# Kernel optimization log

Measured on AMD Instinct MI355X. Metric: run time of the kernel, lower is better.

## Reference

```python
import jax, jax.numpy as jnp
import numpy as np
from functools import partial

B = 1024          # batch of VRP instances
N_CUST = 100      # customers
N = N_CUST + 1    # nodes incl. depot (node 0)
E = 128           # embed_dim
H = 8             # n_heads
DH = E // H       # head depth
CLIP = 10.0
T = 2 * N         # fixed number of decode steps (env.n_nodes * 2)


def setup_inputs() -> dict:
    key = jax.random.key(0)
    ks = jax.random.split(key, 11)
    s = E ** -0.5
    return {
        "depot_xy": jax.random.uniform(ks[0], (B, 2), dtype=jnp.float32),
        "customer_xy": jax.random.uniform(ks[1], (B, N_CUST, 2), dtype=jnp.float32),
        # demands normalized by vehicle capacity (1..9 / 50 for VRP100)
        "demand": jax.random.uniform(ks[2], (B, N_CUST), dtype=jnp.float32, minval=0.02, maxval=0.18),
        "node_embeddings": jax.random.normal(ks[3], (B, N, E), dtype=jnp.float32),
        "graph_embedding": jax.random.normal(ks[4], (B, E), dtype=jnp.float32),
        "Wk1": jax.random.normal(ks[5], (E, E), dtype=jnp.float32) * s,
        "Wv": jax.random.normal(ks[6], (E, E), dtype=jnp.float32) * s,
        "Wk2": jax.random.normal(ks[7], (E, E), dtype=jnp.float32) * s,
        "Wq_fixed": jax.random.normal(ks[8], (E, E), dtype=jnp.float32) * s,
        "Wout": jax.random.normal(ks[9], (E, E), dtype=jnp.float32) * s,
        "Wq_step": jax.random.normal(ks[10], (E + 1, E), dtype=jnp.float32) * s,
    }


def _decode(depot_xy, customer_xy, demand, node_embeddings, graph_embedding,
            Wk1, Wv, Wk2, Wq_fixed, Wout, Wq_step):
    # ---- compute_static ----
    Q_fixed = jnp.einsum('be,ef->bf', graph_embedding, Wq_fixed)[:, None, :]  # [B,1,E]
    K1 = jnp.einsum('bne,ef->bnf', node_embeddings, Wk1)                      # [B,N,E]
    V  = jnp.einsum('bne,ef->bnf', node_embeddings, Wv)
    K2 = jnp.einsum('bne,ef->bnf', node_embeddings, Wk2)
    K1h = K1.reshape(B, N, H, DH)
    Vh  = V.reshape(B, N, H, DH)
    inv_sqrt_dh = 1.0 / np.sqrt(DH)
    inv_sqrt_e = 1.0 / np.sqrt(E)
    bidx = jnp.arange(B)
    NEG = jnp.float32(-1e9)

    def step(carry, _):
        mask, D, prev_node, visited = carry
        # step_context = [embedding of current node, remaining capacity D]
        prev_emb = node_embeddings[bidx, prev_node]                 # [B,E]
        step_context = jnp.concatenate([prev_emb, D], axis=-1)[:, None, :]  # [B,1,E+1]
        # ---- compute_dynamic ----
        Q1 = Q_fixed + jnp.einsum('bqc,cf->bqf', step_context, Wq_step)      # [B,1,E]
        Q1h = Q1.reshape(B, 1, H, DH)
        scores = jnp.einsum('bqhd,bkhd->bhqk', Q1h, K1h) * inv_sqrt_dh       # [B,H,1,N]
        scores = jnp.where(mask[:, None, None, :], NEG, scores)
        attn = jax.nn.softmax(scores, axis=-1)
        glimpse = jnp.einsum('bhqk,bkhd->bqhd', attn, Vh).reshape(B, 1, E)
        Q2 = jnp.einsum('bqe,ef->bqf', glimpse, Wout)                        # [B,1,E]
        logits = CLIP * jnp.tanh(jnp.einsum('bqe,bke->bqk', Q2, K2) * inv_sqrt_e)
        logits = jnp.where(mask[:, None, :], NEG, logits)[:, 0]             # [B,N]
        log_p = jax.nn.log_softmax(logits, axis=-1)
        next_node = jnp.argmax(log_p, axis=-1)                               # greedy decode
        # ---- env._get_step ----
        is_depot = next_node == 0
        cust = jnp.clip(next_node - 1, 0, N_CUST - 1)
        sel_dem = jnp.where(is_depot, 0.0, demand[bidx, cust])
        D_new = jnp.where(is_depot[:, None], 1.0, D - sel_dem[:, None])      # refill at depot
        sel_onehot = (jnp.arange(N_CUST)[None, :] == cust[:, None]) & (~is_depot[:, None])
        visited = visited | sel_onehot
        mask_cust = visited | (demand > D_new)                               # visited or too big
        all_visited = jnp.all(visited, axis=-1)
        mask_depot = is_depot & (~all_visited)                               # can't stay at depot
        mask = jnp.concatenate([mask_depot[:, None], mask_cust], axis=-1)
        return (mask, D_new, next_node, visited), (log_p, next_node)

    mask0 = jnp.concatenate([jnp.ones((B, 1), bool), jnp.zeros((B, N_CUST), bool)], axis=-1)
    D0 = jnp.ones((B, 1), jnp.float32)
    prev0 = jnp.zeros((B,), jnp.int32)
    visited0 = jnp.zeros((B, N_CUST), bool)
    _, (log_ps, tours) = jax.lax.scan(step, (mask0, D0, prev0, visited0), None, length=T)
    log_ps = jnp.transpose(log_ps, (1, 0, 2))   # [B,T,N]
    tours = jnp.transpose(tours, (1, 0))        # [B,T]

    # ---- get_costs ----
    coords = jnp.concatenate([depot_xy[:, None, :], customer_xy], axis=1)    # [B,N,2]
    d = coords[bidx[:, None], tours]                                         # [B,T,2]
    def seglen(v):
        return jnp.sqrt(jnp.sum(v * v, axis=-1) + 1e-10)
    cost = (seglen(d[:, 1:] - d[:, :-1]).sum(-1)
            + seglen(d[:, 0] - depot_xy) + seglen(d[:, -1] - depot_xy))
    # ---- get_log_likelihood ----
    ll = jnp.take_along_axis(log_ps, tours[..., None], axis=-1)[..., 0].sum(-1)
    return cost, ll


def reference(depot_xy, customer_xy, demand, node_embeddings, graph_embedding,
              Wk1, Wv, Wk2, Wq_fixed, Wout, Wq_step):
    return _decode(depot_xy, customer_xy, demand, node_embeddings, graph_embedding,
                   Wk1, Wv, Wk2, Wq_fixed, Wout, Wq_step)
```

## Files before the change

kernel.cpp:

```cpp
#include <hip/hip_runtime.h>
#include <math.h>

#define B_   1024
#define NC   100
#define NN   101
#define E_   128
#define T_   202
#define SVP  132
#define NEGV   -1.0e9
#define GAPTHR 1.0e-3f
#define INVSQE 0.08838834764831845f
#define INVSQED 0.08838834764831845

__device__ __forceinline__ float rdlane(float v, int l) {
    return __int_as_float(__builtin_amdgcn_readlane(__float_as_int(v), l));
}
__device__ __forceinline__ float fast_tanh(float x) {
    float xc = fminf(fmaxf(x, -15.f), 15.f);
    float e  = __expf(2.f * xc);
    return (e - 1.f) / (e + 1.f);
}

__global__ void k_weights(const float* __restrict__ Wk2,
                          const float* __restrict__ Wout,
                          double* __restrict__ M64,
                          float* __restrict__ M32) {
    int g = blockIdx.x;
    int e = threadIdx.x;
    const float* w2 = Wk2 + g * E_;
    const float* wo = Wout + e * E_;
    double acc = 0.0;
#pragma unroll 8
    for (int f = 0; f < E_; ++f) acc += (double)w2[f] * (double)wo[f];
    M64[g * E_ + e] = acc;
    M32[g * E_ + e] = (float)acc;
}

__global__ __launch_bounds__(512, 2)
void k_decode(const float* __restrict__ depot_xy,
              const float* __restrict__ customer_xy,
              const float* __restrict__ demand,
              const float* __restrict__ node_emb,
              const float* __restrict__ graph_emb,
              const float* __restrict__ Wk1,
              const float* __restrict__ Wv,
              const float* __restrict__ Wq_fixed,
              const float* __restrict__ Wq_step,
              const double* __restrict__ M64,
              const float* __restrict__ M32,
              float* __restrict__ out)
{
    __shared__ float  sKs[NN * E_];
    __shared__ __align__(16) float sV[104 * SVP];
    __shared__ double sU[2224];
    __shared__ double sQfix64[E_];
    __shared__ double sWqD64[E_];
    __shared__ float  sQfix32[E_];
    __shared__ float  sWqD32[E_];
    __shared__ float  sCoord[2 * NN];
    __shared__ float  sDem[NC];
    __shared__ float  sD;
    __shared__ double sCost, sLL;
    __shared__ float  sPosX, sPosY;
    __shared__ int    sPrev, sMaskDepot, sTrig, sOvf;
    __shared__ unsigned long long sVis0, sVis1;

    float* fSc  = (float*)sU;
    float* fPx8 = (float*)sU + 832;
    double* dUZ = sU;
    double* dSc = sU + 1024;
    double* dQ1 = sU + 1832;
    double* dGl = sU + 1960;
    double* dVg = sU + 2088;

    const int b      = blockIdx.x;
    const int tid    = threadIdx.x;
    const int lane   = tid & 63;
    const int h      = __builtin_amdgcn_readfirstlane(tid >> 6);
    const int k1     = lane + 64;

    const float* emb = node_emb + (size_t)b * NN * E_;

    if (tid < E_) {
        const float* ge = graph_emb + (size_t)b * E_;
        double acc = 0.0;
        for (int g = 0; g < E_; ++g)
            acc += (double)ge[g] * (double)Wq_fixed[g * E_ + tid];
        sQfix64[tid] = acc;
        sQfix32[tid] = (float)acc;
        sWqD64[tid]  = (double)Wq_step[128 * E_ + tid];
        sWqD32[tid]  = Wq_step[128 * E_ + tid];
    }
    if (tid < 2 * NN) {
        int k = tid >> 1, xy = tid & 1;
        sCoord[tid] = (k == 0) ? depot_xy[(size_t)b * 2 + xy]
                               : customer_xy[((size_t)b * NC + (k - 1)) * 2 + xy];
    }
    if (tid < NC) sDem[tid] = demand[(size_t)b * NC + tid];
    if (tid == 0) {
        sD = 1.f; sPrev = 0; sVis0 = 0ull; sVis1 = 0ull;
        sMaskDepot = 1; sCost = 0.0; sLL = 0.0; sTrig = 0; sOvf = 0;
        sPosX = depot_xy[(size_t)b * 2 + 0];
        sPosY = depot_xy[(size_t)b * 2 + 1];
    }
    for (int i = tid; i < 3 * SVP; i += 512) sV[101 * SVP + i] = 0.f;

    for (int idx = tid; idx < NN * 32; idx += 512) {
        int k  = idx >> 5;
        int e4 = (idx & 31) * 4;
        const float* er = emb + (size_t)k * E_;
        float4 aV = {0.f, 0.f, 0.f, 0.f};
        float4 aK = {0.f, 0.f, 0.f, 0.f};
        for (int g = 0; g < E_; ++g) {
            float eg = er[g];
            float4 wv = *(const float4*)(Wv      + (size_t)g * E_ + e4);
            float4 wq = *(const float4*)(Wq_step + (size_t)g * E_ + e4);
            aV.x += eg * wv.x; aV.y += eg * wv.y;
            aV.z += eg * wv.z; aV.w += eg * wv.w;
            aK.x += eg * wq.x; aK.y += eg * wq.y;
            aK.z += eg * wq.z; aK.w += eg * wq.w;
        }
        *(float4*)(sV  + (size_t)k * SVP + e4) = aV;
        *(float4*)(sKs + (size_t)k * E_  + e4) = aK;
    }

    float rA[32], rK2[32];
#pragma unroll
    for (int j = 0; j < 32; ++j) { rA[j] = 0.f; rK2[j] = 0.f; }
    {
        const float* er0 = emb + (size_t)lane * E_;
        const float* er1 = emb + (size_t)((k1 < NN) ? k1 : lane) * E_;
        const float  e1s = (k1 < NN) ? 1.f : 0.f;
        const float* w1b = Wk1 + h * 16;
        const float* m2b = M32 + h * 16;
        for (int g = 0; g < E_; ++g) {
            float a0 = er0[g];
            float a1 = er1[g] * e1s;
            const float* w1 = w1b + (size_t)g * E_;
            const float* mm = m2b + (size_t)g * E_;
#pragma unroll
            for (int d = 0; d < 16; ++d) {
                rA[d]       += a0 * w1[d];
                rA[16 + d]  += a1 * w1[d];
                rK2[d]      += a0 * mm[d];
                rK2[16 + d] += a1 * mm[d];
            }
        }
    }
    __syncthreads();

    for (int t = 0; t < T_; ++t) {
        {
            int prev = sPrev;
            float Dv = sD;
            int d_ = h * 16 + (lane & 15);
            float q1v = (sQfix32[d_] + sKs[(size_t)prev * E_ + d_]
                         + Dv * sWqD32[d_]) * 0.25f;

            unsigned long long v0 = sVis0, v1 = sVis1;
            bool mk0, mk1;
            if (lane == 0) mk0 = (sMaskDepot != 0);
            else {
                int c = lane - 1;
                mk0 = ((v0 >> c) & 1ull) || (sDem[c] > Dv);
            }
            if (k1 < NN) {
                int c = k1 - 1;
                bool vis = (c < 64) ? ((v0 >> c) & 1ull)
                                    : ((v1 >> (c - 64)) & 1ull);
                mk1 = vis || (sDem[c] > Dv);
            } else mk1 = true;

            float s0a = 0.f, s0b = 0.f, s1a = 0.f, s1b = 0.f;
#pragma unroll
            for (int d = 0; d < 8; ++d) {
                float qd = rdlane(q1v, d);
                s0a += rA[d] * qd;
                s1a += rA[16 + d] * qd;
            }
#pragma unroll
            for (int d = 8; d < 16; ++d) {
                float qd = rdlane(q1v, d);
                s0b += rA[d] * qd;
                s1b += rA[16 + d] * qd;
            }
            float s0 = s0a + s0b, s1 = s1a + s1b;
            bool ovf = (!mk0 && s0 > 80.f) || (!mk1 && s1 > 80.f);
            if (__any(ovf)) { if (lane == 0) sOvf = 1; }
            float w0 = mk0 ? 0.f : __expf(fminf(s0, 80.f));
            float w1 = mk1 ? 0.f : __expf(fminf(s1, 80.f));
            fSc[h * 104 + lane] = w0;
            if (k1 < 104) fSc[h * 104 + k1] = w1;

            __builtin_amdgcn_wave_barrier();

            int cq4 = lane >> 4;
            const float* sc = fSc + h * 104 + cq4 * 26;
            const float* vv = sV + (size_t)(cq4 * 26) * SVP + d_;
            float p = 0.f, ssum = 0.f;
#pragma unroll
            for (int j = 0; j < 26; ++j) {
                float wgt = sc[j];
                p    += wgt * vv[(size_t)j * SVP];
                ssum += wgt;
            }
            p    += __shfl_xor(p, 16);
            ssum += __shfl_xor(ssum, 16);
            p    += __shfl_xor(p, 32);
            ssum += __shfl_xor(ssum, 32);
            float glval = p * (1.0f / ssum);

            float x0 = 0.f, x1 = 0.f;
#pragma unroll
            for (int d = 0; d < 16; ++d) {
                float gd = rdlane(glval, d);
                x0 += rK2[d] * gd;
                x1 += rK2[16 + d] * gd;
            }
            fPx8[h * E_ + lane] = x0;
            if (k1 < NN) fPx8[h * E_ + k1] = x1;
        }
        __syncthreads();

        if (tid < 64) {
            int kA = tid, kB = tid + 64;
            float xA = 0.f, xB = -3.0e38f;
#pragma unroll
            for (int hh = 0; hh < 8; ++hh) xA += fPx8[hh * E_ + kA];
            xA *= INVSQE;
            bool mk1;
            if (kA == 0) mk1 = (sMaskDepot != 0);
            else {
                int c = kA - 1;
                bool vis = (c < 64) ? ((sVis0 >> c) & 1ull) : ((sVis1 >> (c - 64)) & 1ull);
                mk1 = vis || (sDem[c] > sD);
            }
            bool mk2 = true;
            if (kB < NN) {
                float xs = 0.f;
#pragma unroll
                for (int hh = 0; hh < 8; ++hh) xs += fPx8[hh * E_ + kB];
                xB = xs * INVSQE;
                int c = kB - 1;
                bool vis = (c < 64) ? ((sVis0 >> c) & 1ull) : ((sVis1 >> (c - 64)) & 1ull);
                mk2 = vis || (sDem[c] > sD);
            }
            float a1v = mk1 ? -3.0e38f : xA;
            float a2v = mk2 ? -3.0e38f : xB;
            float m1; int mi;
            if (a2v > a1v) { m1 = a2v; mi = kB; }
            else           { m1 = a1v; mi = kA; }
            float ls = 0.f;
            if (!mk1)              ls += __expf(10.f * fast_tanh(xA));
            if (kB < NN && !mk2)   ls += __expf(10.f * fast_tanh(xB));
#pragma unroll
            for (int off = 32; off > 0; off >>= 1) {
                float om1 = __shfl_xor(m1, off);
                int   omi = __shfl_xor(mi, off);
                ls += __shfl_xor(ls, off);
                if (om1 > m1 || (om1 == m1 && omi < mi)) { m1 = om1; mi = omi; }
            }
            bool near = false;
            if (!mk1 && kA != mi && a1v > m1 - GAPTHR) near = true;
            if (!mk2 && kB != mi && a2v > m1 - GAPTHR) near = true;
            bool trigAny = __any(near);
            if (tid == 0) {
                bool trig = trigAny || (sOvf != 0) || !(m1 == m1);
                sOvf = 0;
                if (trig) {
                    sTrig = 1;
                } else {
                    float lsel = 10.f * fast_tanh(m1);
                    float logp = lsel - __logf(ls);
                    int nxt = mi;
                    sLL += (double)logp;
                    bool isdep = (nxt == 0);
                    if (isdep) {
                        sD = 1.0f;
                    } else {
                        int c = nxt - 1;
                        sD = sD - sDem[c];
                        if (c < 64) sVis0 |= (1ull << c);
                        else        sVis1 |= (1ull << (c - 64));
                    }
                    bool allv = (sVis0 == 0xFFFFFFFFFFFFFFFFull) &&
                                (sVis1 == 0x0000000FFFFFFFFFull);
                    sMaskDepot = (isdep && !allv) ? 1 : 0;
                    sPrev = nxt;
                    float cx = sCoord[2 * nxt], cy = sCoord[2 * nxt + 1];
                    double dx = (double)cx - (double)sPosX;
                    double dy = (double)cy - (double)sPosY;
                    sCost += sqrt(dx * dx + dy * dy + 1e-10);
                    sPosX = cx; sPosY = cy;
                }
            }
        }
        __syncthreads();

        if (sTrig) {
            if (tid < E_) {
                const float* ep = emb + (size_t)sPrev * E_;
                double ks = 0.0;
                for (int g = 0; g < E_; ++g)
                    ks += (double)ep[g] * (double)Wq_step[(size_t)g * E_ + tid];
                dQ1[tid] = (sQfix64[tid] + ks + (double)sD * sWqD64[tid]) * 0.25;
            }
            __syncthreads();
            for (int idx = tid; idx < 1024; idx += 512) {
                int g = idx >> 3, hh = idx & 7;
                double u = 0.0;
#pragma unroll 4
                for (int d = 0; d < 16; ++d)
                    u += dQ1[hh * 16 + d] * (double)Wk1[(size_t)g * E_ + hh * 16 + d];
                dUZ[idx] = u;
            }
            __syncthreads();
            for (int idx = tid; idx < 1024; idx += 512) {
                int k = idx & 127, hh = idx >> 7;
                if (k < NN) {
                    bool mk;
                    if (k == 0) mk = (sMaskDepot != 0);
                    else {
                        int c = k - 1;
                        bool vis = (c < 64) ? ((sVis0 >> c) & 1ull) : ((sVis1 >> (c - 64)) & 1ull);
                        mk = vis || (sDem[c] > sD);
                    }
                    if (mk) dSc[hh * NN + k] = NEGV;
                    else {
                        const float* ek = emb + (size_t)k * E_;
                        double s = 0.0;
                        for (int g = 0; g < E_; ++g)
                            s += (double)ek[g] * dUZ[g * 8 + hh];
                        dSc[hh * NN + k] = s;
                    }
                }
            }
            __syncthreads();
            {
                int hh = tid >> 6, ln = tid & 63;
                int kA = ln, kB = ln + 64;
                double v1 = dSc[hh * NN + kA];
                double v2 = (kB < NN) ? dSc[hh * NN + kB] : -1.0e300;
                double m = fmax(v1, v2);
#pragma unroll
                for (int off = 32; off > 0; off >>= 1)
                    m = fmax(m, __shfl_xor(m, off));
                double e1 = exp(v1 - m);
                double e2 = (kB < NN) ? exp(v2 - m) : 0.0;
                double s = e1 + e2;
#pragma unroll
                for (int off = 32; off > 0; off >>= 1)
                    s += __shfl_xor(s, off);
                double inv = 1.0 / s;
                dSc[hh * NN + kA] = e1 * inv;
                if (kB < NN) dSc[hh * NN + kB] = e2 * inv;
            }
            __syncthreads();
            for (int idx = tid; idx < 1024; idx += 512) {
                int g = idx >> 3, hh = idx & 7;
                double z = 0.0;
                for (int k = 0; k < NN; ++k)
                    z += dSc[hh * NN + k] * (double)emb[(size_t)k * E_ + g];
                dUZ[idx] = z;
            }
            __syncthreads();
            if (tid < E_) {
                int hh = tid >> 4;
                double g2 = 0.0;
                for (int g = 0; g < E_; ++g)
                    g2 += dUZ[g * 8 + hh] * (double)Wv[(size_t)g * E_ + tid];
                dGl[tid] = g2;
            }
            __syncthreads();
            if (tid < E_) {
                double v = 0.0;
                for (int e = 0; e < E_; ++e)
                    v += dGl[e] * M64[(size_t)tid * E_ + e];
                dVg[tid] = v;
            }
            __syncthreads();
            if (tid < NN) {
                const float* ek = emb + (size_t)tid * E_;
                double x = 0.0;
                for (int g = 0; g < E_; ++g)
                    x += (double)ek[g] * dVg[g];
                dQ1[tid] = x * INVSQED;
            }
            __syncthreads();
            if (tid < 64) {
                int kA = tid, kB = tid + 64;
                double x1 = dQ1[kA];
                bool mk1;
                if (kA == 0) mk1 = (sMaskDepot != 0);
                else {
                    int c = kA - 1;
                    bool vis = (c < 64) ? ((sVis0 >> c) & 1ull) : ((sVis1 >> (c - 64)) & 1ull);
                    mk1 = vis || (sDem[c] > sD);
                }
                double x2 = 0.0; bool mk2 = true;
                if (kB < NN) {
                    x2 = dQ1[kB];
                    int c = kB - 1;
                    bool vis = (c < 64) ? ((sVis0 >> c) & 1ull) : ((sVis1 >> (c - 64)) & 1ull);
                    mk2 = vis || (sDem[c] > sD);
                }
                double a1 = mk1 ? -1.0e300 : x1;
                double a2 = (kB < NN && !mk2) ? x2 : -1.0e300;
                double mv; int mi;
                if (a1 >= a2) { mv = a1; mi = kA; } else { mv = a2; mi = kB; }
#pragma unroll
                for (int off = 32; off > 0; off >>= 1) {
                    double ov = __shfl_xor(mv, off);
                    int    oi = __shfl_xor(mi, off);
                    if (ov > mv || (ov == mv && oi < mi)) { mv = ov; mi = oi; }
                }
                double lmax = 10.0 * tanh(mv);
                double l1 = mk1 ? NEGV : 10.0 * tanh(x1);
                double l2 = (kB < NN) ? (mk2 ? NEGV : 10.0 * tanh(x2)) : 0.0;
                double s = exp(l1 - lmax) + ((kB < NN) ? exp(l2 - lmax) : 0.0);
#pragma unroll
                for (int off = 32; off > 0; off >>= 1)
                    s += __shfl_xor(s, off);
                if (tid == 0) {
                    int nxt = mi;
                    sLL += -log(s);
                    bool isdep = (nxt == 0);
                    if (isdep) {
                        sD = 1.0f;
                    } else {
                        int c = nxt - 1;
                        sD = sD - sDem[c];
                        if (c < 64) sVis0 |= (1ull << c);
                        else        sVis1 |= (1ull << (c - 64));
                    }
                    bool allv = (sVis0 == 0xFFFFFFFFFFFFFFFFull) &&
                                (sVis1 == 0x0000000FFFFFFFFFull);
                    sMaskDepot = (isdep && !allv) ? 1 : 0;
                    sPrev = nxt;
                    float cx = sCoord[2 * nxt], cy = sCoord[2 * nxt + 1];
                    double dx = (double)cx - (double)sPosX;
                    double dy = (double)cy - (double)sPosY;
                    sCost += sqrt(dx * dx + dy * dy + 1e-10);
                    sPosX = cx; sPosY = cy;
                    sTrig = 0;
                }
            }
            __syncthreads();
        }
    }

    if (tid == 0) {
        double dx = (double)sCoord[0] - (double)sPosX;
        double dy = (double)sCoord[1] - (double)sPosY;
        out[b]      = (float)(sCost + sqrt(dx * dx + dy * dy + 1e-10));
        out[B_ + b] = (float)sLL;
    }
}

extern "C" void kernel_launch(void* const* d_in, const int* in_sizes, int n_in,
                              void* d_out, int out_size, void* d_ws, size_t ws_size,
                              hipStream_t stream) {
    const float* depot = (const float*)d_in[0];
    const float* cust  = (const float*)d_in[1];
    const float* dem   = (const float*)d_in[2];
    const float* nemb  = (const float*)d_in[3];
    const float* gemb  = (const float*)d_in[4];
    const float* Wk1   = (const float*)d_in[5];
    const float* Wv    = (const float*)d_in[6];
    const float* Wk2   = (const float*)d_in[7];
    const float* Wqf   = (const float*)d_in[8];
    const float* Wout  = (const float*)d_in[9];
    const float* Wqs   = (const float*)d_in[10];
    float*  out = (float*)d_out;
    double* M64 = (double*)d_ws;
    float*  M32 = (float*)((char*)d_ws + 131072);

    k_weights<<<dim3(128), dim3(128), 0, stream>>>(Wk2, Wout, M64, M32);
    k_decode <<<dim3(B_),  dim3(512), 0, stream>>>(depot, cust, dem, nemb, gemb,
                                                   Wk1, Wv, Wqf, Wqs, M64, M32, out);
}
```

Before: 3.130 ms.

## Replicate decode state in registers and drop per-step barrier via double buffering

Every wave now redundantly computes the argmax/selection and keeps the decode state (capacity, visited bits, prev node, cost, log-likelihood) in registers, instead of wave 0 updating shared memory and all waves re-reading it after a second barrier. Per-step partial logits and overflow flags are double-buffered by step parity, so each step needs only one __syncthreads on the fast path. The slow fp64 fallback is kept, now nested inside the branch, with state copied to and from shared memory. The trade is redundant selection work in all eight waves and a larger reduction per wave, in exchange for removing a block-wide barrier and the shared-memory state round trip each step.

```diff
diff --git a/kernel.cpp b/kernel.cpp
--- a/kernel.cpp
+++ b/kernel.cpp
@@ -62,22 +62,23 @@
     __shared__ float  sD;
     __shared__ double sCost, sLL;
     __shared__ float  sPosX, sPosY;
-    __shared__ int    sPrev, sMaskDepot, sTrig, sOvf;
+    __shared__ int    sPrev, sMaskDepot, sTrig;
     __shared__ unsigned long long sVis0, sVis1;
 
     float* fSc  = (float*)sU;
-    float* fPx8 = (float*)sU + 832;
+    float* fPxD = (float*)sU + 832;
+    int*   sOvfA = (int*)((float*)sU + 2880);
     double* dUZ = sU;
     double* dSc = sU + 1024;
     double* dQ1 = sU + 1832;
     double* dGl = sU + 1960;
     double* dVg = sU + 2088;
 
-    const int b      = blockIdx.x;
-    const int tid    = threadIdx.x;
-    const int lane   = tid & 63;
-    const int h      = __builtin_amdgcn_readfirstlane(tid >> 6);
-    const int k1     = lane + 64;
+    const int b    = blockIdx.x;
+    const int tid  = threadIdx.x;
+    const int lane = tid & 63;
+    const int h    = __builtin_amdgcn_readfirstlane(tid >> 6);
+    const int k1   = lane + 64;
 
     const float* emb = node_emb + (size_t)b * NN * E_;
 
@@ -97,12 +98,7 @@
                                : customer_xy[((size_t)b * NC + (k - 1)) * 2 + xy];
     }
     if (tid < NC) sDem[tid] = demand[(size_t)b * NC + tid];
-    if (tid == 0) {
-        sD = 1.f; sPrev = 0; sVis0 = 0ull; sVis1 = 0ull;
-        sMaskDepot = 1; sCost = 0.0; sLL = 0.0; sTrig = 0; sOvf = 0;
-        sPosX = depot_xy[(size_t)b * 2 + 0];
-        sPosY = depot_xy[(size_t)b * 2 + 1];
-    }
+    if (tid == 0) sTrig = 0;
     for (int i = tid; i < 3 * SVP; i += 512) sV[101 * SVP + i] = 0.f;
 
     for (int idx = tid; idx < NN * 32; idx += 512) {
@@ -147,27 +143,33 @@
             }
         }
     }
+
+    float  rD = 1.0f;
+    int    rPrev = 0, rMaskDep = 1;
+    unsigned long long rV0 = 0ull, rV1 = 0ull;
+    double rCost = 0.0, rLL = 0.0;
+    float  rPx = depot_xy[(size_t)b * 2 + 0];
+    float  rPy = depot_xy[(size_t)b * 2 + 1];
     __syncthreads();
 
     for (int t = 0; t < T_; ++t) {
+        const int bsel = t & 1;
         {
-            int prev = sPrev;
-            float Dv = sD;
+            float Dv = rD;
             int d_ = h * 16 + (lane & 15);
-            float q1v = (sQfix32[d_] + sKs[(size_t)prev * E_ + d_]
+            float q1v = (sQfix32[d_] + sKs[(size_t)rPrev * E_ + d_]
                          + Dv * sWqD32[d_]) * 0.25f;
 
-            unsigned long long v0 = sVis0, v1 = sVis1;
             bool mk0, mk1;
-            if (lane == 0) mk0 = (sMaskDepot != 0);
+            if (lane == 0) mk0 = (rMaskDep != 0);
             else {
                 int c = lane - 1;
-                mk0 = ((v0 >> c) & 1ull) || (sDem[c] > Dv);
+                mk0 = ((rV0 >> c) & 1ull) || (sDem[c] > Dv);
             }
             if (k1 < NN) {
                 int c = k1 - 1;
-                bool vis = (c < 64) ? ((v0 >> c) & 1ull)
-                                    : ((v1 >> (c - 64)) & 1ull);
+                bool vis = (c < 64) ? ((rV0 >> c) & 1ull)
+                                    : ((rV1 >> (c - 64)) & 1ull);
                 mk1 = vis || (sDem[c] > Dv);
             } else mk1 = true;
 
@@ -186,7 +188,8 @@
             }
             float s0 = s0a + s0b, s1 = s1a + s1b;
             bool ovf = (!mk0 && s0 > 80.f) || (!mk1 && s1 > 80.f);
-            if (__any(ovf)) { if (lane == 0) sOvf = 1; }
+            int wOvf = __any(ovf) ? 1 : 0;
+            if (lane == 0) sOvfA[bsel * 8 + h] = wOvf;
             float w0 = mk0 ? 0.f : __expf(fminf(s0, 80.f));
             float w1 = mk1 ? 0.f : __expf(fminf(s1, 80.f));
             fSc[h * 104 + lane] = w0;
@@ -217,34 +220,40 @@
                 x0 += rK2[d] * gd;
                 x1 += rK2[16 + d] * gd;
             }
-            fPx8[h * E_ + lane] = x0;
-            if (k1 < NN) fPx8[h * E_ + k1] = x1;
+            float* px = fPxD + bsel * 1024 + h * E_;
+            px[lane] = x0;
+            if (k1 < NN) px[k1] = x1;
         }
         __syncthreads();
 
-        if (tid < 64) {
-            int kA = tid, kB = tid + 64;
-            float xA = 0.f, xB = -3.0e38f;
-#pragma unroll
-            for (int hh = 0; hh < 8; ++hh) xA += fPx8[hh * E_ + kA];
+        {
+            int kA = lane, kB = k1;
+            const float* px = fPxD + bsel * 1024;
+            float xA = 0.f;
+#pragma unroll
+            for (int hh = 0; hh < 8; ++hh) xA += px[hh * E_ + kA];
             xA *= INVSQE;
             bool mk1;
-            if (kA == 0) mk1 = (sMaskDepot != 0);
+            if (kA == 0) mk1 = (rMaskDep != 0);
             else {
                 int c = kA - 1;
-                bool vis = (c < 64) ? ((sVis0 >> c) & 1ull) : ((sVis1 >> (c - 64)) & 1ull);
-                mk1 = vis || (sDem[c] > sD);
-            }
-            bool mk2 = true;
+                bool vis = (c < 64) ? ((rV0 >> c) & 1ull) : ((rV1 >> (c - 64)) & 1ull);
+                mk1 = vis || (sDem[c] > rD);
+            }
+            float xB = -3.0e38f; bool mk2 = true;
             if (kB < NN) {
                 float xs = 0.f;
 #pragma unroll
-                for (int hh = 0; hh < 8; ++hh) xs += fPx8[hh * E_ + kB];
+                for (int hh = 0; hh < 8; ++hh) xs += px[hh * E_ + kB];
                 xB = xs * INVSQE;
                 int c = kB - 1;
-                bool vis = (c < 64) ? ((sVis0 >> c) & 1ull) : ((sVis1 >> (c - 64)) & 1ull);
-                mk2 = vis || (sDem[c] > sD);
-            }
+                bool vis = (c < 64) ? ((rV0 >> c) & 1ull) : ((rV1 >> (c - 64)) & 1ull);
+                mk2 = vis || (sDem[c] > rD);
+            }
+            int oa = 0;
+#pragma unroll
+            for (int hh = 0; hh < 8; ++hh) oa |= sOvfA[bsel * 8 + hh];
+
             float a1v = mk1 ? -3.0e38f : xA;
             float a2v = mk2 ? -3.0e38f : xB;
             float m1; int mi;
@@ -264,196 +273,199 @@
             if (!mk1 && kA != mi && a1v > m1 - GAPTHR) near = true;
             if (!mk2 && kB != mi && a2v > m1 - GAPTHR) near = true;
             bool trigAny = __any(near);
-            if (tid == 0) {
-                bool trig = trigAny || (sOvf != 0) || !(m1 == m1);
-                sOvf = 0;
-                if (trig) {
+            bool trig = trigAny || (oa != 0) || !(m1 == m1);
+
+            if (!trig) {
+                int nxt = mi;
+                float lsel = 10.f * fast_tanh(m1);
+                float logp = lsel - __logf(ls);
+                rLL += (double)logp;
+                bool isdep = (nxt == 0);
+                if (isdep) {
+                    rD = 1.0f;
+                } else {
+                    int c = nxt - 1;
+                    rD = rD - sDem[c];
+                    if (c < 64) rV0 |= (1ull << c);
+                    else        rV1 |= (1ull << (c - 64));
+                }
+                bool allv = (rV0 == 0xFFFFFFFFFFFFFFFFull) &&
+                            (rV1 == 0x0000000FFFFFFFFFull);
+                rMaskDep = (isdep && !allv) ? 1 : 0;
+                rPrev = nxt;
+                float cx = sCoord[2 * nxt], cy = sCoord[2 * nxt + 1];
+                double dx = (double)cx - (double)rPx;
+                double dy = (double)cy - (double)rPy;
+                rCost += sqrt(dx * dx + dy * dy + 1e-10);
+                rPx = cx; rPy = cy;
+            } else {
+                if (tid == 0) {
+                    sD = rD; sPrev = rPrev; sMaskDepot = rMaskDep;
+                    sVis0 = rV0; sVis1 = rV1;
+                    sCost = rCost; sLL = rLL; sPosX = rPx; sPosY = rPy;
                     sTrig = 1;
-                } else {
-                    float lsel = 10.f * fast_tanh(m1);
-                    float logp = lsel - __logf(ls);
-                    int nxt = mi;
-                    sLL += (double)logp;
-                    bool isdep = (nxt == 0);
-                    if (isdep) {
-                        sD = 1.0f;
-                    } else {
-                        int c = nxt - 1;
-                        sD = sD - sDem[c];
-                        if (c < 64) sVis0 |= (1ull << c);
-                        else        sVis1 |= (1ull << (c - 64));
+                }
+                __syncthreads();
+                if (tid < E_) {
+                    const float* ep = emb + (size_t)sPrev * E_;
+                    double ks = 0.0;
+                    for (int g = 0; g < E_; ++g)
+                        ks += (double)ep[g] * (double)Wq_step[(size_t)g * E_ + tid];
+                    dQ1[tid] = (sQfix64[tid] + ks + (double)sD * sWqD64[tid]) * 0.25;
+                }
+                __syncthreads();
+                for (int idx = tid; idx < 1024; idx += 512) {
+                    int g = idx >> 3, hh = idx & 7;
+                    double u = 0.0;
+#pragma unroll 4
+                    for (int d = 0; d < 16; ++d)
+                        u += dQ1[hh * 16 + d] * (double)Wk1[(size_t)g * E_ + hh * 16 + d];
+                    dUZ[idx] = u;
+                }
+                __syncthreads();
+                for (int idx = tid; idx < 1024; idx += 512) {
+                    int k = idx & 127, hh = idx >> 7;
+                    if (k < NN) {
+                        bool mk;
+                        if (k == 0) mk = (sMaskDepot != 0);
+                        else {
+                            int c = k - 1;
+                            bool vis = (c < 64) ? ((sVis0 >> c) & 1ull) : ((sVis1 >> (c - 64)) & 1ull);
+                            mk = vis || (sDem[c] > sD);
+                        }
+                        if (mk) dSc[hh * NN + k] = NEGV;
+                        else {
+                            const float* ek = emb + (size_t)k * E_;
+                            double s = 0.0;
+                            for (int g = 0; g < E_; ++g)
+                                s += (double)ek[g] * dUZ[g * 8 + hh];
+                            dSc[hh * NN + k] = s;
+                        }
                     }
-                    bool allv = (sVis0 == 0xFFFFFFFFFFFFFFFFull) &&
-                                (sVis1 == 0x0000000FFFFFFFFFull);
-                    sMaskDepot = (isdep && !allv) ? 1 : 0;
-                    sPrev = nxt;
-                    float cx = sCoord[2 * nxt], cy = sCoord[2 * nxt + 1];
-                    double dx = (double)cx - (double)sPosX;
-                    double dy = (double)cy - (double)sPosY;
-                    sCost += sqrt(dx * dx + dy * dy + 1e-10);
-                    sPosX = cx; sPosY = cy;
-                }
+                }
+                __syncthreads();
+                {
+                    int hh = tid >> 6, ln = tid & 63;
+                    int kA2 = ln, kB2 = ln + 64;
+                    double v1 = dSc[hh * NN + kA2];
+                    double v2 = (kB2 < NN) ? dSc[hh * NN + kB2] : -1.0e300;
+                    double m = fmax(v1, v2);
+#pragma unroll
+                    for (int off = 32; off > 0; off >>= 1)
+                        m = fmax(m, __shfl_xor(m, off));
+                    double e1 = exp(v1 - m);
+                    double e2 = (kB2 < NN) ? exp(v2 - m) : 0.0;
+                    double s = e1 + e2;
+#pragma unroll
+                    for (int off = 32; off > 0; off >>= 1)
+                        s += __shfl_xor(s, off);
+                    double inv = 1.0 / s;
+                    dSc[hh * NN + kA2] = e1 * inv;
+                    if (kB2 < NN) dSc[hh * NN + kB2] = e2 * inv;
+                }
+                __syncthreads();
+                for (int idx = tid; idx < 1024; idx += 512) {
+                    int g = idx >> 3, hh = idx & 7;
+                    double z = 0.0;
+                    for (int k = 0; k < NN; ++k)
+                        z += dSc[hh * NN + k] * (double)emb[(size_t)k * E_ + g];
+                    dUZ[idx] = z;
+                }
+                __syncthreads();
+                if (tid < E_) {
+                    int hh = tid >> 4;
+                    double g2 = 0.0;
+                    for (int g = 0; g < E_; ++g)
+                        g2 += dUZ[g * 8 + hh] * (double)Wv[(size_t)g * E_ + tid];
+                    dGl[tid] = g2;
+                }
+                __syncthreads();
+                if (tid < E_) {
+                    double v = 0.0;
+                    for (int e = 0; e < E_; ++e)
+                        v += dGl[e] * M64[(size_t)tid * E_ + e];
+                    dVg[tid] = v;
+                }
+                __syncthreads();
+                if (tid < NN) {
+                    const float* ek = emb + (size_t)tid * E_;
+                    double x = 0.0;
+                    for (int g = 0; g < E_; ++g)
+                        x += (double)ek[g] * dVg[g];
+                    dQ1[tid] = x * INVSQED;
+                }
+                __syncthreads();
+                if (tid < 64) {
+                    int kA2 = tid, kB2 = tid + 64;
+                    double x1 = dQ1[kA2];
+                    bool fk1;
+                    if (kA2 == 0) fk1 = (sMaskDepot != 0);
+                    else {
+                        int c = kA2 - 1;
+                        bool vis = (c < 64) ? ((sVis0 >> c) & 1ull) : ((sVis1 >> (c - 64)) & 1ull);
+                        fk1 = vis || (sDem[c] > sD);
+                    }
+                    double x2 = 0.0; bool fk2 = true;
+                    if (kB2 < NN) {
+                        x2 = dQ1[kB2];
+                        int c = kB2 - 1;
+                        bool vis = (c < 64) ? ((sVis0 >> c) & 1ull) : ((sVis1 >> (c - 64)) & 1ull);
+                        fk2 = vis || (sDem[c] > sD);
+                    }
+                    double a1 = fk1 ? -1.0e300 : x1;
+                    double a2 = (kB2 < NN && !fk2) ? x2 : -1.0e300;
+                    double mv; int fmi;
+                    if (a1 >= a2) { mv = a1; fmi = kA2; } else { mv = a2; fmi = kB2; }
+#pragma unroll
+                    for (int off = 32; off > 0; off >>= 1) {
+                        double ov = __shfl_xor(mv, off);
+                        int    oi = __shfl_xor(fmi, off);
+                        if (ov > mv || (ov == mv && oi < fmi)) { mv = ov; fmi = oi; }
+                    }
+                    double lmax = 10.0 * tanh(mv);
+                    double l1 = fk1 ? NEGV : 10.0 * tanh(x1);
+                    double l2 = (kB2 < NN) ? (fk2 ? NEGV : 10.0 * tanh(x2)) : 0.0;
+                    double s = exp(l1 - lmax) + ((kB2 < NN) ? exp(l2 - lmax) : 0.0);
+#pragma unroll
+                    for (int off = 32; off > 0; off >>= 1)
+                        s += __shfl_xor(s, off);
+                    if (tid == 0) {
+                        int nxt = fmi;
+                        sLL += -log(s);
+                        bool isdep = (nxt == 0);
+                        if (isdep) {
+                            sD = 1.0f;
+                        } else {
+                            int c = nxt - 1;
+                            sD = sD - sDem[c];
+                            if (c < 64) sVis0 |= (1ull << c);
+                            else        sVis1 |= (1ull << (c - 64));
+                        }
+                        bool allv = (sVis0 == 0xFFFFFFFFFFFFFFFFull) &&
+                                    (sVis1 == 0x0000000FFFFFFFFFull);
+                        sMaskDepot = (isdep && !allv) ? 1 : 0;
+                        sPrev = nxt;
+                        float cx = sCoord[2 * nxt], cy = sCoord[2 * nxt + 1];
+                        double dx = (double)cx - (double)sPosX;
+                        double dy = (double)cy - (double)sPosY;
+                        sCost += sqrt(dx * dx + dy * dy + 1e-10);
+                        sPosX = cx; sPosY = cy;
+                        sTrig = 0;
+                    }
+                }
+                __syncthreads();
+                rD = sD; rPrev = sPrev; rMaskDep = sMaskDepot;
+                rV0 = sVis0; rV1 = sVis1;
+                rCost = sCost; rLL = sLL; rPx = sPosX; rPy = sPosY;
             }
         }
-        __syncthreads();
-
-        if (sTrig) {
-            if (tid < E_) {
-                const float* ep = emb + (size_t)sPrev * E_;
-                double ks = 0.0;
-                for (int g = 0; g < E_; ++g)
-                    ks += (double)ep[g] * (double)Wq_step[(size_t)g * E_ + tid];
-                dQ1[tid] = (sQfix64[tid] + ks + (double)sD * sWqD64[tid]) * 0.25;
-            }
-            __syncthreads();
-            for (int idx = tid; idx < 1024; idx += 512) {
-                int g = idx >> 3, hh = idx & 7;
-                double u = 0.0;
-#pragma unroll 4
-                for (int d = 0; d < 16; ++d)
-                    u += dQ1[hh * 16 + d] * (double)Wk1[(size_t)g * E_ + hh * 16 + d];
-                dUZ[idx] = u;
-            }
-            __syncthreads();
-            for (int idx = tid; idx < 1024; idx += 512) {
-                int k = idx & 127, hh = idx >> 7;
-                if (k < NN) {
-                    bool mk;
-                    if (k == 0) mk = (sMaskDepot != 0);
-                    else {
-                        int c = k - 1;
-                        bool vis = (c < 64) ? ((sVis0 >> c) & 1ull) : ((sVis1 >> (c - 64)) & 1ull);
-                        mk = vis || (sDem[c] > sD);
-                    }
-                    if (mk) dSc[hh * NN + k] = NEGV;
-                    else {
-                        const float* ek = emb + (size_t)k * E_;
-                        double s = 0.0;
-                        for (int g = 0; g < E_; ++g)
-                            s += (double)ek[g] * dUZ[g * 8 + hh];
-                        dSc[hh * NN + k] = s;
-                    }
-                }
-            }
-            __syncthreads();
-            {
-                int hh = tid >> 6, ln = tid & 63;
-                int kA = ln, kB = ln + 64;
-                double v1 = dSc[hh * NN + kA];
-                double v2 = (kB < NN) ? dSc[hh * NN + kB] : -1.0e300;
-                double m = fmax(v1, v2);
-#pragma unroll
-                for (int off = 32; off > 0; off >>= 1)
-                    m = fmax(m, __shfl_xor(m, off));
-                double e1 = exp(v1 - m);
-                double e2 = (kB < NN) ? exp(v2 - m) : 0.0;
-                double s = e1 + e2;
-#pragma unroll
-                for (int off = 32; off > 0; off >>= 1)
-                    s += __shfl_xor(s, off);
-                double inv = 1.0 / s;
-                dSc[hh * NN + kA] = e1 * inv;
-                if (kB < NN) dSc[hh * NN + kB] = e2 * inv;
-            }
-            __syncthreads();
-            for (int idx = tid; idx < 1024; idx += 512) {
-                int g = idx >> 3, hh = idx & 7;
-                double z = 0.0;
-                for (int k = 0; k < NN; ++k)
-                    z += dSc[hh * NN + k] * (double)emb[(size_t)k * E_ + g];
-                dUZ[idx] = z;
-            }
-            __syncthreads();
-            if (tid < E_) {
-                int hh = tid >> 4;
-                double g2 = 0.0;
-                for (int g = 0; g < E_; ++g)
-                    g2 += dUZ[g * 8 + hh] * (double)Wv[(size_t)g * E_ + tid];
-                dGl[tid] = g2;
-            }
-            __syncthreads();
-            if (tid < E_) {
-                double v = 0.0;
-                for (int e = 0; e < E_; ++e)
-                    v += dGl[e] * M64[(size_t)tid * E_ + e];
-                dVg[tid] = v;
-            }
-            __syncthreads();
-            if (tid < NN) {
-                const float* ek = emb + (size_t)tid * E_;
-                double x = 0.0;
-                for (int g = 0; g < E_; ++g)
-                    x += (double)ek[g] * dVg[g];
-                dQ1[tid] = x * INVSQED;
-            }
-            __syncthreads();
-            if (tid < 64) {
-                int kA = tid, kB = tid + 64;
-                double x1 = dQ1[kA];
-                bool mk1;
-                if (kA == 0) mk1 = (sMaskDepot != 0);
-                else {
-                    int c = kA - 1;
-                    bool vis = (c < 64) ? ((sVis0 >> c) & 1ull) : ((sVis1 >> (c - 64)) & 1ull);
-                    mk1 = vis || (sDem[c] > sD);
-                }
-                double x2 = 0.0; bool mk2 = true;
-                if (kB < NN) {
-                    x2 = dQ1[kB];
-                    int c = kB - 1;
-                    bool vis = (c < 64) ? ((sVis0 >> c) & 1ull) : ((sVis1 >> (c - 64)) & 1ull);
-                    mk2 = vis || (sDem[c] > sD);
-                }
-                double a1 = mk1 ? -1.0e300 : x1;
-                double a2 = (kB < NN && !mk2) ? x2 : -1.0e300;
-                double mv; int mi;
-                if (a1 >= a2) { mv = a1; mi = kA; } else { mv = a2; mi = kB; }
-#pragma unroll
-                for (int off = 32; off > 0; off >>= 1) {
-                    double ov = __shfl_xor(mv, off);
-                    int    oi = __shfl_xor(mi, off);
-                    if (ov > mv || (ov == mv && oi < mi)) { mv = ov; mi = oi; }
-                }
-                double lmax = 10.0 * tanh(mv);
-                double l1 = mk1 ? NEGV : 10.0 * tanh(x1);
-                double l2 = (kB < NN) ? (mk2 ? NEGV : 10.0 * tanh(x2)) : 0.0;
-                double s = exp(l1 - lmax) + ((kB < NN) ? exp(l2 - lmax) : 0.0);
-#pragma unroll
-                for (int off = 32; off > 0; off >>= 1)
-                    s += __shfl_xor(s, off);
-                if (tid == 0) {
-                    int nxt = mi;
-                    sLL += -log(s);
-                    bool isdep = (nxt == 0);
-                    if (isdep) {
-                        sD = 1.0f;
-                    } else {
-                        int c = nxt - 1;
-                        sD = sD - sDem[c];
-                        if (c < 64) sVis0 |= (1ull << c);
-                        else        sVis1 |= (1ull << (c - 64));
-                    }
-                    bool allv = (sVis0 == 0xFFFFFFFFFFFFFFFFull) &&
-                                (sVis1 == 0x0000000FFFFFFFFFull);
-                    sMaskDepot = (isdep && !allv) ? 1 : 0;
-                    sPrev = nxt;
-                    float cx = sCoord[2 * nxt], cy = sCoord[2 * nxt + 1];
-                    double dx = (double)cx - (double)sPosX;
-                    double dy = (double)cy - (double)sPosY;
-                    sCost += sqrt(dx * dx + dy * dy + 1e-10);
-                    sPosX = cx; sPosY = cy;
-                    sTrig = 0;
-                }
-            }
-            __syncthreads();
-        }
     }
 
     if (tid == 0) {
-        double dx = (double)sCoord[0] - (double)sPosX;
-        double dy = (double)sCoord[1] - (double)sPosY;
-        out[b]      = (float)(sCost + sqrt(dx * dx + dy * dy + 1e-10));
-        out[B_ + b] = (float)sLL;
+        double dx = (double)sCoord[0] - (double)rPx;
+        double dy = (double)sCoord[1] - (double)rPy;
+        out[b]      = (float)(rCost + sqrt(dx * dx + dy * dy + 1e-10));
+        out[B_ + b] = (float)rLL;
     }
 }
 
```

New measurement: 3.012 ms. 3.8% less time.
